# Performance work log

Measured on AMD Instinct MI355X. Metric: run time of the kernel, lower is better.

The kernel has to match this reference:

```python
import jax, jax.numpy as jnp
import numpy as np
import math

B, T, C, H, L, V = 8, 511, 1024, 16, 8, 128  # T = block_size - 1
D = C // H
FF = 4 * C


def setup_inputs() -> dict:
    key = jax.random.key(0)
    ks = jax.random.split(key, 12)
    std = 0.02
    n = lambda k, s: (jax.random.normal(k, s, dtype=jnp.float32) * std)
    idx = jax.random.randint(ks[0], (B, T), 0, V)
    idx = jnp.where(idx == 2, 3, idx)  # avoid pad token so logits[idx!=2] keeps all rows
    return {
        "idx": idx,
        "tok_emb": n(ks[1], (V, C)),
        "pos_emb": n(ks[2], (T, C)),
        "ln1_w": jnp.ones((L, C)), "ln1_b": jnp.zeros((L, C)),
        "Wq": n(ks[3], (L, C, C)), "bq": jnp.zeros((L, C)),
        "Wk": n(ks[4], (L, C, C)), "bk": jnp.zeros((L, C)),
        "Wv": n(ks[5], (L, C, C)), "bv": jnp.zeros((L, C)),
        "Wp": n(ks[6], (L, C, C)), "bp": jnp.zeros((L, C)),
        "ln2_w": jnp.ones((L, C)), "ln2_b": jnp.zeros((L, C)),
        "W1": n(ks[7], (L, C, FF)), "b1": jnp.zeros((L, FF)),
        "W2": n(ks[8], (L, FF, C)), "b2": jnp.zeros((L, C)),
        "lnf_w": jnp.ones((C,)), "lnf_b": jnp.zeros((C,)),
        "head_w": n(ks[9], (V, C)),
    }


def _ln(x, w, b):
    m = x.mean(-1, keepdims=True)
    v = ((x - m) ** 2).mean(-1, keepdims=True)
    return (x - m) * jax.lax.rsqrt(v + 1e-5) * w + b


def reference(idx, tok_emb, pos_emb, ln1_w, ln1_b, Wq, bq, Wk, bk, Wv, bv, Wp, bp,
              ln2_w, ln2_b, W1, b1, W2, b2, lnf_w, lnf_b, head_w):
    x = tok_emb[idx] + pos_emb[None, :, :]                      # [B,T,C]
    mask = jnp.tril(jnp.ones((T, T), dtype=bool))
    scale = 1.0 / math.sqrt(D)

    def block(x, p):
        h = _ln(x, p["ln1_w"], p["ln1_b"])
        q = (h @ p["Wq"] + p["bq"]).reshape(B, T, H, D).transpose(0, 2, 1, 3)
        k = (h @ p["Wk"] + p["bk"]).reshape(B, T, H, D).transpose(0, 2, 1, 3)
        v = (h @ p["Wv"] + p["bv"]).reshape(B, T, H, D).transpose(0, 2, 1, 3)
        att = jnp.einsum('bhqd,bhkd->bhqk', q, k) * scale       # [B,H,T,T]
        att = jnp.where(mask, att, -jnp.inf)
        att = jax.nn.softmax(att, axis=-1)
        y = jnp.einsum('bhqk,bhkd->bhqd', att, v)
        y = y.transpose(0, 2, 1, 3).reshape(B, T, C)
        x = x + y @ p["Wp"] + p["bp"]
        h = _ln(x, p["ln2_w"], p["ln2_b"])
        h = jax.nn.gelu(h @ p["W1"] + p["b1"], approximate=False)
        x = x + h @ p["W2"] + p["b2"]
        return x, None

    stacked = dict(ln1_w=ln1_w, ln1_b=ln1_b, Wq=Wq, bq=bq, Wk=Wk, bk=bk, Wv=Wv, bv=bv,
                   Wp=Wp, bp=bp, ln2_w=ln2_w, ln2_b=ln2_b, W1=W1, b1=b1, W2=W2, b2=b2)
    x, _ = jax.lax.scan(block, x, stacked)
    x = _ln(x, lnf_w, lnf_b)
    logits = x @ head_w.T                                       # [B,T,V]
    # logits[idx != 2] with no 2-tokens present == all rows flattened
    return logits.reshape(B * T, V)
```

## Files before the change

kernel.cpp:

```cpp
#include <hip/hip_runtime.h>
#include <hip/hip_bf16.h>

typedef unsigned short u16;
typedef unsigned int   u32;
typedef __attribute__((ext_vector_type(8))) __bf16 bf16x8;
typedef __attribute__((ext_vector_type(4))) float  f32x4;

static constexpr int NB  = 8;
static constexpr int TT  = 511;
static constexpr int CC  = 1024;
static constexpr int HH  = 16;
static constexpr int LL  = 8;
static constexpr int VV  = 128;
static constexpr int FF_ = 4096;
static constexpr int MV  = NB * TT;
static constexpr int MP  = 4096;
static constexpr int TP  = 512;

#define DEVI static __device__ __forceinline__

DEVI u16 f2bf(float f) {
  u32 u = __builtin_bit_cast(u32, f);
  u = (u + 0x7fffu + ((u >> 16) & 1u)) >> 16;
  return (u16)u;
}

DEVI void gload16(const void* g, void* lds) {
  auto gp = (const __attribute__((address_space(1))) u32*)(uintptr_t)g;
  auto lp = (__attribute__((address_space(3))) u32*)(uintptr_t)lds;
  __builtin_amdgcn_global_load_lds(gp, lp, 16, 0, 0);
}

__global__ __launch_bounds__(256) void k_transpose(const float* __restrict__ in,
                                                   u16* __restrict__ out, int K, int N,
                                                   size_t is, size_t os) {
  in  += (size_t)blockIdx.z * is;
  out += (size_t)blockIdx.z * os;
  __shared__ u16 tile[64][66];
  int nb = blockIdx.x * 64, kb = blockIdx.y * 64;
  int t = threadIdx.x;
  int r = t >> 4, c4 = (t & 15) * 4;
#pragma unroll
  for (int i = 0; i < 4; ++i) {
    int k = r + i * 16;
    float4 v = *(const float4*)(in + (size_t)(kb + k) * N + nb + c4);
    tile[k][c4 + 0] = f2bf(v.x); tile[k][c4 + 1] = f2bf(v.y);
    tile[k][c4 + 2] = f2bf(v.z); tile[k][c4 + 3] = f2bf(v.w);
  }
  __syncthreads();
#pragma unroll
  for (int i = 0; i < 4; ++i) {
    int n = r + i * 16;
    ushort4 o;
    o.x = tile[c4 + 0][n]; o.y = tile[c4 + 1][n];
    o.z = tile[c4 + 2][n]; o.w = tile[c4 + 3][n];
    *(ushort4*)(out + (size_t)(nb + n) * K + kb + c4) = o;
  }
}

__global__ __launch_bounds__(256) void k_transpose4(const float* __restrict__ Wq,
                                                    const float* __restrict__ Wk,
                                                    const float* __restrict__ Wv,
                                                    const float* __restrict__ Wp,
                                                    u16* __restrict__ wqkv_t,
                                                    u16* __restrict__ wp_t) {
  int z = blockIdx.z, which = z >> 3, lyr = z & 7;
  const float* in; u16* out;
  size_t sq = (size_t)CC * CC;
  if (which == 0)      { in = Wq + lyr * sq; out = wqkv_t + lyr * 3 * sq; }
  else if (which == 1) { in = Wk + lyr * sq; out = wqkv_t + lyr * 3 * sq + sq; }
  else if (which == 2) { in = Wv + lyr * sq; out = wqkv_t + lyr * 3 * sq + 2 * sq; }
  else                 { in = Wp + lyr * sq; out = wp_t + lyr * sq; }
  __shared__ u16 tile[64][66];
  int nb = blockIdx.x * 64, kb = blockIdx.y * 64;
  int t = threadIdx.x;
  int r = t >> 4, c4 = (t & 15) * 4;
#pragma unroll
  for (int i = 0; i < 4; ++i) {
    int k = r + i * 16;
    float4 v = *(const float4*)(in + (size_t)(kb + k) * CC + nb + c4);
    tile[k][c4 + 0] = f2bf(v.x); tile[k][c4 + 1] = f2bf(v.y);
    tile[k][c4 + 2] = f2bf(v.z); tile[k][c4 + 3] = f2bf(v.w);
  }
  __syncthreads();
#pragma unroll
  for (int i = 0; i < 4; ++i) {
    int n = r + i * 16;
    ushort4 o;
    o.x = tile[c4 + 0][n]; o.y = tile[c4 + 1][n];
    o.z = tile[c4 + 2][n]; o.w = tile[c4 + 3][n];
    *(ushort4*)(out + (size_t)(nb + n) * CC + kb + c4) = o;
  }
}

__global__ __launch_bounds__(256) void k_prep(const float* __restrict__ headw,
                                              const float* __restrict__ bq,
                                              const float* __restrict__ bk,
                                              const float* __restrict__ bv,
                                              u16* __restrict__ headb,
                                              float* __restrict__ bqkv) {
  int i = blockIdx.x * 256 + threadIdx.x;
  if (i < VV * CC) {
    headb[i] = f2bf(headw[i]);
  } else {
    int j = i - VV * CC;
    if (j < LL * 3 * CC) {
      int l = j / (3 * CC), c = j % (3 * CC);
      float v = (c < CC) ? bq[l * CC + c] : (c < 2 * CC) ? bk[l * CC + c - CC] : bv[l * CC + c - 2 * CC];
      bqkv[j] = v;
    }
  }
}

__global__ __launch_bounds__(256) void k_embed(const int* __restrict__ idx,
                                               const float* __restrict__ tok,
                                               const float* __restrict__ pos,
                                               float* __restrict__ x) {
  int row = blockIdx.x;
  int c4 = threadIdx.x * 4;
  if (row >= MV) {
    *(float4*)(x + (size_t)row * CC + c4) = make_float4(0.f, 0.f, 0.f, 0.f);
    return;
  }
  int t = row % TT;
  int tid = idx[row];
  float4 a = *(const float4*)(tok + (size_t)tid * CC + c4);
  float4 p = *(const float4*)(pos + (size_t)t * CC + c4);
  a.x += p.x; a.y += p.y; a.z += p.z; a.w += p.w;
  *(float4*)(x + (size_t)row * CC + c4) = a;
}

__global__ __launch_bounds__(256) void k_ln(const float* __restrict__ x,
                                            const float* __restrict__ w,
                                            const float* __restrict__ b,
                                            u16* __restrict__ out) {
  int wid = threadIdx.x >> 6, l = threadIdx.x & 63;
  int row = blockIdx.x * 4 + wid;
  const float* xr = x + (size_t)row * CC;
  float4 v[4];
  float s = 0.f, sq = 0.f;
#pragma unroll
  for (int i = 0; i < 4; ++i) {
    v[i] = *(const float4*)(xr + (i * 64 + l) * 4);
    s  += v[i].x + v[i].y + v[i].z + v[i].w;
    sq += v[i].x * v[i].x + v[i].y * v[i].y + v[i].z * v[i].z + v[i].w * v[i].w;
  }
#pragma unroll
  for (int o = 32; o; o >>= 1) { s += __shfl_xor(s, o); sq += __shfl_xor(sq, o); }
  float mean = s * (1.f / CC);
  float var  = sq * (1.f / CC) - mean * mean;
  float rs = rsqrtf(var + 1e-5f);
#pragma unroll
  for (int i = 0; i < 4; ++i) {
    int c = (i * 64 + l) * 4;
    float4 wv = *(const float4*)(w + c);
    float4 bv = *(const float4*)(b + c);
    ushort4 o4;
    o4.x = f2bf((v[i].x - mean) * rs * wv.x + bv.x);
    o4.y = f2bf((v[i].y - mean) * rs * wv.y + bv.y);
    o4.z = f2bf((v[i].z - mean) * rs * wv.z + bv.z);
    o4.w = f2bf((v[i].w - mean) * rs * wv.w + bv.w);
    *(ushort4*)(out + (size_t)row * CC + c) = o4;
  }
}

template <int EPI>
__global__ __launch_bounds__(512, 1) void k_gemm4(const u16* __restrict__ A,
                                                  const u16* __restrict__ Wt,
                                                  const float* __restrict__ bias,
                                                  u16* __restrict__ outb,
                                                  u16* __restrict__ vt,
                                                  int N, int K, int gridN) {
  __shared__ char lds[2][4][16384];
  int t = threadIdx.x, l = t & 63, wid = t >> 6;
  int wr = wid >> 2, wc = wid & 3;
  int lr = l & 15, lk16 = (l >> 4) * 16;

  int nwg = gridDim.x, wg = blockIdx.x;
  int qq = nwg >> 3, r8 = nwg & 7;
  int xcd = wg & 7, loc = wg >> 3;
  int swz = (xcd < r8 ? xcd * (qq + 1) : r8 * (qq + 1) + (xcd - r8) * qq) + loc;
  int mblk = swz / gridN, nblk = swz - mblk * gridN;
  int mb = mblk * 256, nb = nblk * 256;
  int NT = K >> 6;
  const u16* Ab = A  + (size_t)mb * K;
  const u16* Bb = Wt + (size_t)nb * K;

  int srow = t >> 3, skb = (t & 7) * 16;

  auto stageH = [&](int kt, int ht) {
    int b = kt & 1;
    const u16* src = (ht < 2) ? Ab : Bb;
    int rowbase = (ht & 1) << 7;
    char* dst = &lds[b][ht][0];
    const u16* s0 = src + (size_t)rowbase * K + kt * 64;
#pragma unroll
    for (int j = 0; j < 2; ++j) {
      int row = j * 64 + srow;
      int kb = skb ^ ((row & 7) << 4);
      gload16(s0 + (size_t)row * K + (kb >> 1), dst + j * 8192 + t * 16);
    }
  };

  f32x4 acc[8][4] = {};

  stageH(0, 0); stageH(0, 1); stageH(0, 2); stageH(0, 3);
  stageH(1, 2); stageH(1, 0); stageH(1, 3);
  asm volatile("s_waitcnt vmcnt(6)" ::: "memory");
  __builtin_amdgcn_s_barrier();
  __builtin_amdgcn_sched_barrier(0);

  for (int kt = 0; kt < NT; kt += 2) {
    bool s2 = (kt + 2) < NT, s3 = (kt + 3) < NT;
#pragma unroll
    for (int half = 0; half < 2; ++half) {
      int buf = half;
      bf16x8 Bf[2][4];
#pragma unroll
      for (int q = 0; q < 4; ++q) {
        bf16x8 Af[2][2];
        if (q == 0) {
#pragma unroll
          for (int ks = 0; ks < 2; ++ks)
#pragma unroll
            for (int nf = 0; nf < 4; ++nf) {
              int grow = ((wc & 1) << 6) + nf * 16 + lr;
              int kb = (ks * 64 + lk16) ^ ((grow & 7) << 4);
              Bf[ks][nf] = *(const bf16x8*)(&lds[buf][2 + (wc >> 1)][0] + grow * 128 + kb);
            }
        }
#pragma unroll
        for (int ks = 0; ks < 2; ++ks)
#pragma unroll
          for (int dm = 0; dm < 2; ++dm) {
            int mf = q * 2 + dm;
            int grow = wr * 64 + (mf & 3) * 16 + lr;
            int kb = (ks * 64 + lk16) ^ ((grow & 7) << 4);
            Af[ks][dm] = *(const bf16x8*)(&lds[buf][mf >> 2][0] + grow * 128 + kb);
          }
        if (half == 0) {
          if (q == 0)      stageH(kt + 1, 1);
          else if (q == 1) { if (s2) stageH(kt + 2, 2); }
          else if (q == 2) { if (s2) stageH(kt + 2, 0); }
          else             { if (s2) stageH(kt + 2, 3); }
        } else {
          if (q == 0)      { if (s2) stageH(kt + 2, 1); }
          else if (q == 1) { if (s3) stageH(kt + 3, 2); }
          else if (q == 2) { if (s3) stageH(kt + 3, 0); }
          else             { if (s3) stageH(kt + 3, 3); }
        }
        __builtin_amdgcn_sched_barrier(0);
        __builtin_amdgcn_s_barrier();
        asm volatile("s_waitcnt lgkmcnt(0)" ::: "memory");
        __builtin_amdgcn_sched_barrier(0);
        __builtin_amdgcn_s_setprio(1);
#pragma unroll
        for (int ks = 0; ks < 2; ++ks)
#pragma unroll
          for (int dm = 0; dm < 2; ++dm)
#pragma unroll
            for (int nf = 0; nf < 4; ++nf)
              acc[q * 2 + dm][nf] = __builtin_amdgcn_mfma_f32_16x16x32_bf16(
                  Af[ks][dm], Bf[ks][nf], acc[q * 2 + dm][nf], 0, 0, 0);
        __builtin_amdgcn_s_setprio(0);
        if (q == 3) {
          if (half == 0) {
            if (s2) asm volatile("s_waitcnt vmcnt(6)" ::: "memory");
            else    asm volatile("s_waitcnt vmcnt(0)" ::: "memory");
          } else if (s2) {
            if (s3) asm volatile("s_waitcnt vmcnt(6)" ::: "memory");
            else    asm volatile("s_waitcnt vmcnt(0)" ::: "memory");
          }
        }
        __builtin_amdgcn_sched_barrier(0);
        __builtin_amdgcn_s_barrier();
      }
    }
  }

  int r0 = (l >> 4) * 4;
#pragma unroll
  for (int mf = 0; mf < 8; ++mf) {
    int gr = mb + ((mf >> 2) << 7) + wr * 64 + (mf & 3) * 16 + r0;
#pragma unroll
    for (int nf = 0; nf < 4; ++nf) {
      int gc = nb + wc * 64 + nf * 16 + lr;
      float bv = bias[gc];
      if constexpr (EPI == 1) {
        if (gc >= 2048) {
          int h = (gc - 2048) >> 6, d = gc & 63;
#pragma unroll
          for (int rr = 0; rr < 4; ++rr) {
            int grow = gr + rr;
            if (grow < MV) {
              int b = grow / TT;
              int tt2 = grow - b * TT;
              vt[(((size_t)(b * HH + h)) * 64 + d) * TP + tt2] = f2bf(acc[mf][nf][rr] + bv);
            }
          }
          continue;
        }
      }
#pragma unroll
      for (int rr = 0; rr < 4; ++rr) {
        float v = acc[mf][nf][rr] + bv;
        size_t o = (size_t)(gr + rr) * N + gc;
        if constexpr (EPI == 1) {
          outb[o] = f2bf(v);
        } else {
          float g = 0.5f * v * (1.0f + erff(v * 0.70710678f));
          outb[o] = f2bf(g);
        }
      }
    }
  }
}

template <int EPI>
__global__ __launch_bounds__(256, 2) void k_gemm3(const u16* __restrict__ A,
                                                  const u16* __restrict__ Wt,
                                                  const float* __restrict__ bias,
                                                  float* __restrict__ outf,
                                                  const float* __restrict__ resid,
                                                  int N, int K, int gridN, int Mv) {
  constexpr int BTILE = 16384;
  __shared__ u16 lds[2][128 * 64 * 2];

  int t = threadIdx.x, l = t & 63, wid = t >> 6;
  int wr = wid >> 1, wc = wid & 1;
  int lr = l & 15, lk16 = (l >> 4) * 16;

  int nwg = gridDim.x, wg = blockIdx.x;
  int q = nwg >> 3, r = nwg & 7;
  int xcd = wg & 7, loc = wg >> 3;
  int swz = (xcd < r ? xcd * (q + 1) : r * (q + 1) + (xcd - r) * q) + loc;
  int mblk = swz / gridN;
  int nblk = swz - mblk * gridN;
  int mb = mblk * 128, nb = nblk * 128;
  int NT = K >> 6;
  const u16* Ab = A  + (size_t)mb * K;
  const u16* Bb = Wt + (size_t)nb * K;

  int srow = t >> 3;
  int skb  = (t & 7) * 16;

  auto stage = [&](int kt, int b) {
    const u16* As = Ab + kt * 64;
    char* LD = (char*)&lds[b][0];
#pragma unroll
    for (int j = 0; j < 4; ++j) {
      int row = j * 32 + srow;
      int kb  = skb ^ ((row & 7) << 4);
      gload16(As + (size_t)row * K + (kb >> 1), LD + j * 4096 + t * 16);
    }
    const u16* Bs = Bb + kt * 64;
#pragma unroll
    for (int j = 0; j < 4; ++j) {
      int row = j * 32 + srow;
      int kb  = skb ^ ((row & 7) << 4);
      gload16(Bs + (size_t)row * K + (kb >> 1), LD + BTILE + j * 4096 + t * 16);
    }
  };

  f32x4 acc[4][4] = {};

  auto tile = [&](int b) {
    const char* LA = (const char*)&lds[b][0];
    const char* LB = LA + BTILE;
    bf16x8 bfr[2][4], afr[2][4];
#pragma unroll
    for (int ks = 0; ks < 2; ++ks)
#pragma unroll
      for (int n = 0; n < 4; ++n) {
        int rr = wc * 64 + n * 16 + lr;
        int kb = (ks * 64 + lk16) ^ ((rr & 7) << 4);
        bfr[ks][n] = *(const bf16x8*)(LB + rr * 128 + kb);
      }
#pragma unroll
    for (int ks = 0; ks < 2; ++ks)
#pragma unroll
      for (int m = 0; m < 4; ++m) {
        int rr = wr * 64 + m * 16 + lr;
        int kb = (ks * 64 + lk16) ^ ((rr & 7) << 4);
        afr[ks][m] = *(const bf16x8*)(LA + rr * 128 + kb);
      }
    __builtin_amdgcn_s_setprio(1);
#pragma unroll
    for (int ks = 0; ks < 2; ++ks)
#pragma unroll
      for (int m = 0; m < 4; ++m)
#pragma unroll
        for (int n = 0; n < 4; ++n)
          acc[m][n] = __builtin_amdgcn_mfma_f32_16x16x32_bf16(
              afr[ks][m], bfr[ks][n], acc[m][n], 0, 0, 0);
    __builtin_amdgcn_s_setprio(0);
  };

  stage(0, 0);
  stage(1, 1);
  asm volatile("s_waitcnt vmcnt(8)" ::: "memory");
  __builtin_amdgcn_s_barrier();
  __builtin_amdgcn_sched_barrier(0);

  for (int kt = 0; kt < NT; kt += 2) {
#pragma unroll
    for (int sub = 0; sub < 2; ++sub) {
      tile(sub);
      asm volatile("s_waitcnt lgkmcnt(0)" ::: "memory");
      __builtin_amdgcn_s_barrier();
      __builtin_amdgcn_sched_barrier(0);
      if (kt + 2 + sub < NT) {
        stage(kt + 2 + sub, sub);
        asm volatile("s_waitcnt vmcnt(8)" ::: "memory");
      } else {
        asm volatile("s_waitcnt vmcnt(0)" ::: "memory");
      }
      __builtin_amdgcn_s_barrier();
      __builtin_amdgcn_sched_barrier(0);
    }
  }

  int r0 = (l >> 4) * 4;
#pragma unroll
  for (int m = 0; m < 4; ++m) {
    int gr = mb + wr * 64 + m * 16 + r0;
#pragma unroll
    for (int n = 0; n < 4; ++n) {
      int gc = nb + wc * 64 + n * 16 + lr;
      float bv = 0.f;
      if constexpr (EPI == 0) bv = bias[gc];
#pragma unroll
      for (int rr = 0; rr < 4; ++rr) {
        int grr = gr + rr;
        float v = acc[m][n][rr] + bv;
        size_t o = (size_t)grr * N + gc;
        if constexpr (EPI == 0) {
          outf[o] = v + resid[o];
        } else {
          if (grr < Mv) outf[o] = v;
        }
      }
    }
  }
}

__global__ __launch_bounds__(512, 2) void k_attn2(const u16* __restrict__ qkv,
                                                  const u16* __restrict__ vt,
                                                  u16* __restrict__ y) {
  __shared__ u16 Kb[2][64 * 64];
  __shared__ u16 Vb[2][64 * 64];
  __shared__ u16 Pb[8][16 * 64];
  int t = threadIdx.x, l = t & 63, w = t >> 6;

  int nwg = gridDim.x, wg = blockIdx.x;
  int swz = (wg & 7) * (nwg >> 3) + (wg >> 3);
  int bh = swz >> 2, qt = swz & 3;
  int b = bh >> 4, h = bh & 15;
  int q0 = qt * 128;
  int lr = l & 15, lg = l >> 4, lk8 = lg * 8;

  const float ISC = 0.125f;

  bf16x8 Qa[2];
  {
    int qs = q0 + w * 16 + lr;
    const u16* qp = qkv + (size_t)(b * TT + (qs < TT ? qs : TT - 1)) * 3072 + h * 64;
    Qa[0] = *(const bf16x8*)(qp + lk8);
    Qa[1] = *(const bf16x8*)(qp + 32 + lk8);
  }

  int NT = (q0 + 128) >> 6;

  int srow = w * 8 + (l >> 3);
  int sb16 = (l & 7) * 16;
  int bcol = sb16 ^ ((srow & 7) << 4);
  const u16* Ksrc = qkv + 1024 + h * 64;
  const char* Vsrc = (const char*)(vt + ((size_t)bh * 64 + srow) * TP);

  auto stage = [&](int kt, int buf) {
    int kv0 = kt * 64;
    int kvr = kv0 + srow;
    int krow = b * TT + (kvr < TT ? kvr : TT - 1);
    gload16((const char*)(Ksrc + (size_t)krow * 3072) + bcol, (char*)&Kb[buf][0] + t * 16);
    gload16(Vsrc + kv0 * 2 + bcol, (char*)&Vb[buf][0] + t * 16);
  };

  f32x4 O[4] = {};
  float m_[4], s_[4];
#pragma unroll
  for (int r = 0; r < 4; ++r) { m_[r] = -1e30f; s_[r] = 0.f; }

  stage(0, 0);
  for (int kt = 0; kt < NT; ++kt) {
    int buf = kt & 1;
    if (kt + 1 < NT) {
      stage(kt + 1, buf ^ 1);
      asm volatile("s_waitcnt vmcnt(2)" ::: "memory");
    } else {
      asm volatile("s_waitcnt vmcnt(0)" ::: "memory");
    }
    __builtin_amdgcn_s_barrier();

    int kv0 = kt * 64;
    f32x4 S[4];
    const char* LK = (const char*)&Kb[buf][0];
#pragma unroll
    for (int j = 0; j < 4; ++j) {
      f32x4 a = {};
#pragma unroll
      for (int ks = 0; ks < 2; ++ks) {
        int row = j * 16 + lr;
        int kb = ((ks * 32 + lk8) * 2) ^ ((row & 7) << 4);
        bf16x8 kf = *(const bf16x8*)(LK + row * 128 + kb);
        a = __builtin_amdgcn_mfma_f32_16x16x32_bf16(Qa[ks], kf, a, 0, 0, 0);
      }
      S[j] = a;
    }
    int qbase = q0 + w * 16 + lg * 4;
#pragma unroll
    for (int j = 0; j < 4; ++j) {
      int kv = kv0 + j * 16 + lr;
#pragma unroll
      for (int r = 0; r < 4; ++r) {
        bool valid = (kv <= qbase + r) && (kv < TT);
        S[j][r] = valid ? S[j][r] : -1e30f;
      }
    }
    float mx[4];
#pragma unroll
    for (int r = 0; r < 4; ++r)
      mx[r] = fmaxf(fmaxf(S[0][r], S[1][r]), fmaxf(S[2][r], S[3][r]));
#pragma unroll
    for (int r = 0; r < 4; ++r) {
      mx[r] = fmaxf(mx[r], __shfl_xor(mx[r], 1));
      mx[r] = fmaxf(mx[r], __shfl_xor(mx[r], 2));
      mx[r] = fmaxf(mx[r], __shfl_xor(mx[r], 4));
      mx[r] = fmaxf(mx[r], __shfl_xor(mx[r], 8));
    }
    float sc[4];
#pragma unroll
    for (int r = 0; r < 4; ++r) {
      float mn = fmaxf(m_[r], mx[r]);
      sc[r] = __expf((m_[r] - mn) * ISC);
      m_[r] = mn;
      s_[r] *= sc[r];
    }
#pragma unroll
    for (int j = 0; j < 4; ++j)
#pragma unroll
      for (int r = 0; r < 4; ++r) O[j][r] *= sc[r];
    float rs[4] = {0.f, 0.f, 0.f, 0.f};
    char* LP = (char*)&Pb[w][0];
#pragma unroll
    for (int j = 0; j < 4; ++j) {
#pragma unroll
      for (int r = 0; r < 4; ++r) {
        float p = __expf((S[j][r] - m_[r]) * ISC);
        rs[r] += p;
        int row = lg * 4 + r;
        int addr = (row * 128 + (j * 16 + lr) * 2) ^ ((row & 7) << 4);
        *(u16*)(LP + addr) = f2bf(p);
      }
    }
#pragma unroll
    for (int r = 0; r < 4; ++r) {
      rs[r] += __shfl_xor(rs[r], 1);
      rs[r] += __shfl_xor(rs[r], 2);
      rs[r] += __shfl_xor(rs[r], 4);
      rs[r] += __shfl_xor(rs[r], 8);
      s_[r] += rs[r];
    }
    bf16x8 Pa[2];
#pragma unroll
    for (int ks = 0; ks < 2; ++ks) {
      int addr = (lr * 128 + (ks * 32 + lk8) * 2) ^ ((lr & 7) << 4);
      Pa[ks] = *(const bf16x8*)(LP + addr);
    }
    const char* LV = (const char*)&Vb[buf][0];
#pragma unroll
    for (int j = 0; j < 4; ++j) {
#pragma unroll
      for (int ks = 0; ks < 2; ++ks) {
        int row = j * 16 + lr;
        int kb = ((ks * 32 + lk8) * 2) ^ ((row & 7) << 4);
        bf16x8 vf = *(const bf16x8*)(LV + row * 128 + kb);
        O[j] = __builtin_amdgcn_mfma_f32_16x16x32_bf16(Pa[ks], vf, O[j], 0, 0, 0);
      }
    }
    asm volatile("s_waitcnt lgkmcnt(0)" ::: "memory");
    __builtin_amdgcn_s_barrier();
  }

  int qs0 = q0 + w * 16 + lg * 4;
#pragma unroll
  for (int r = 0; r < 4; ++r) {
    float inv = 1.0f / s_[r];
    int qs = qs0 + r;
    if (qs < TT) {
      u16* yp = y + (size_t)(b * TT + qs) * CC + h * 64;
#pragma unroll
      for (int j = 0; j < 4; ++j)
        yp[j * 16 + lr] = f2bf(O[j][r] * inv);
    }
  }
}

extern "C" void kernel_launch(void* const* d_in, const int* in_sizes, int n_in,
                              void* d_out, int out_size, void* d_ws, size_t ws_size,
                              hipStream_t stream) {
  (void)in_sizes; (void)n_in; (void)out_size; (void)ws_size;
  const int*   idx  = (const int*)  d_in[0];
  const float* tok  = (const float*)d_in[1];
  const float* pos  = (const float*)d_in[2];
  const float* ln1w = (const float*)d_in[3];
  const float* ln1b = (const float*)d_in[4];
  const float* Wq   = (const float*)d_in[5];
  const float* bq   = (const float*)d_in[6];
  const float* Wk   = (const float*)d_in[7];
  const float* bk   = (const float*)d_in[8];
  const float* Wv   = (const float*)d_in[9];
  const float* bv   = (const float*)d_in[10];
  const float* Wp   = (const float*)d_in[11];
  const float* bp   = (const float*)d_in[12];
  const float* ln2w = (const float*)d_in[13];
  const float* ln2b = (const float*)d_in[14];
  const float* W1   = (const float*)d_in[15];
  const float* b1   = (const float*)d_in[16];
  const float* W2   = (const float*)d_in[17];
  const float* b2   = (const float*)d_in[18];
  const float* lnfw = (const float*)d_in[19];
  const float* lnfb = (const float*)d_in[20];
  const float* headw= (const float*)d_in[21];
  float* out = (float*)d_out;

  char* p = (char*)d_ws;
  auto alloc = [&](size_t bytes) { char* r = p; p += (bytes + 255) & ~(size_t)255; return r; };
  u16*   wqkv_t = (u16*)  alloc((size_t)LL * 3 * CC * CC * 2);
  u16*   wp_t   = (u16*)  alloc((size_t)LL * CC * CC * 2);
  u16*   w1_t   = (u16*)  alloc((size_t)LL * FF_ * CC * 2);
  u16*   w2_t   = (u16*)  alloc((size_t)LL * CC * FF_ * 2);
  u16*   headb  = (u16*)  alloc((size_t)VV * CC * 2);
  float* bqkv   = (float*)alloc((size_t)LL * 3 * CC * 4);
  float* x      = (float*)alloc((size_t)MP * CC * 4);
  u16*   hbuf   = (u16*)  alloc((size_t)MP * CC * 2);
  u16*   qkv    = (u16*)  alloc((size_t)MP * 3 * CC * 2);
  u16*   vt     = (u16*)  alloc((size_t)NB * HH * 64 * TP * 2);
  u16*   ybuf   = (u16*)  alloc((size_t)MP * CC * 2);
  u16*   ffb    = (u16*)  alloc((size_t)MP * FF_ * 2);

  k_transpose4<<<dim3(16, 16, 4 * LL), 256, 0, stream>>>(Wq, Wk, Wv, Wp, wqkv_t, wp_t);
  k_transpose<<<dim3(64, 16, LL), 256, 0, stream>>>(W1, w1_t, CC, FF_, (size_t)CC * FF_, (size_t)FF_ * CC);
  k_transpose<<<dim3(16, 64, LL), 256, 0, stream>>>(W2, w2_t, FF_, CC, (size_t)FF_ * CC, (size_t)CC * FF_);
  k_prep<<<(VV * CC + LL * 3 * CC + 255) / 256, 256, 0, stream>>>(headw, bq, bk, bv, headb, bqkv);

  k_embed<<<MP, 256, 0, stream>>>(idx, tok, pos, x);

  for (int l = 0; l < LL; ++l) {
    k_ln<<<MP / 4, 256, 0, stream>>>(x, ln1w + (size_t)l * CC, ln1b + (size_t)l * CC, hbuf);
    k_gemm4<1><<<12 * 16, 512, 0, stream>>>(hbuf, wqkv_t + (size_t)l * 3 * CC * CC,
                                            bqkv + (size_t)l * 3 * CC, qkv, vt, 3 * CC, CC, 12);
    k_attn2<<<NB * HH * 4, 512, 0, stream>>>(qkv, vt, ybuf);
    k_gemm3<0><<<32 * 8, 256, 0, stream>>>(ybuf, wp_t + (size_t)l * CC * CC,
                                           bp + (size_t)l * CC, x, x, CC, CC, 8, MP);
    k_ln<<<MP / 4, 256, 0, stream>>>(x, ln2w + (size_t)l * CC, ln2b + (size_t)l * CC, hbuf);
    k_gemm4<2><<<16 * 16, 512, 0, stream>>>(hbuf, w1_t + (size_t)l * FF_ * CC,
                                            b1 + (size_t)l * FF_, ffb, nullptr, FF_, CC, 16);
    k_gemm3<0><<<32 * 8, 256, 0, stream>>>(ffb, w2_t + (size_t)l * CC * FF_,
                                           b2 + (size_t)l * CC, x, x, CC, FF_, 8, MP);
  }

  k_ln<<<MP / 4, 256, 0, stream>>>(x, lnfw, lnfb, hbuf);
  k_gemm3<3><<<32 * 1, 256, 0, stream>>>(hbuf, headb, nullptr, out, nullptr, VV, CC, 1, MV);
}
```

Baseline: 1.840 ms.

## Split-K head GEMM, separate V transpose kernel, wider transpose stores

Replaces the 32-block head GEMM with an 8-way split-K GEMM that writes fp32 partials to a workspace buffer, followed by a reduction kernel. This fills more CUs for the small final projection. It also moves the scattered V-transpose writes out of the QKV GEMM epilogue into a dedicated LDS-tiled transpose kernel. The weight transpose kernels now store 16 bytes per thread instead of 8. These changes add extra launches and partial-buffer traffic, and the split-K path falls back to the old kernel if the workspace is too small.

```diff
diff --git a/kernel.cpp b/kernel.cpp
--- a/kernel.cpp
+++ b/kernel.cpp
@@ -5,6 +5,7 @@
 typedef unsigned int   u32;
 typedef __attribute__((ext_vector_type(8))) __bf16 bf16x8;
 typedef __attribute__((ext_vector_type(4))) float  f32x4;
+typedef __attribute__((ext_vector_type(8))) unsigned short u16x8;
 
 static constexpr int NB  = 8;
 static constexpr int TT  = 511;
@@ -16,6 +17,7 @@
 static constexpr int MV  = NB * TT;
 static constexpr int MP  = 4096;
 static constexpr int TP  = 512;
+static constexpr size_t PH = (size_t)MP * VV;
 
 #define DEVI static __device__ __forceinline__
 
@@ -48,13 +50,14 @@
     tile[k][c4 + 2] = f2bf(v.z); tile[k][c4 + 3] = f2bf(v.w);
   }
   __syncthreads();
-#pragma unroll
-  for (int i = 0; i < 4; ++i) {
-    int n = r + i * 16;
-    ushort4 o;
-    o.x = tile[c4 + 0][n]; o.y = tile[c4 + 1][n];
-    o.z = tile[c4 + 2][n]; o.w = tile[c4 + 3][n];
-    *(ushort4*)(out + (size_t)(nb + n) * K + kb + c4) = o;
+  int k8 = (t & 7) * 8;
+#pragma unroll
+  for (int i = 0; i < 2; ++i) {
+    int n = (t >> 3) + i * 32;
+    u16x8 o;
+#pragma unroll
+    for (int j = 0; j < 8; ++j) o[j] = tile[k8 + j][n];
+    *(u16x8*)(out + (size_t)(nb + n) * K + kb + k8) = o;
   }
 }
 
@@ -83,13 +86,14 @@
     tile[k][c4 + 2] = f2bf(v.z); tile[k][c4 + 3] = f2bf(v.w);
   }
   __syncthreads();
-#pragma unroll
-  for (int i = 0; i < 4; ++i) {
-    int n = r + i * 16;
-    ushort4 o;
-    o.x = tile[c4 + 0][n]; o.y = tile[c4 + 1][n];
-    o.z = tile[c4 + 2][n]; o.w = tile[c4 + 3][n];
-    *(ushort4*)(out + (size_t)(nb + n) * CC + kb + c4) = o;
+  int k8 = (t & 7) * 8;
+#pragma unroll
+  for (int i = 0; i < 2; ++i) {
+    int n = (t >> 3) + i * 32;
+    u16x8 o;
+#pragma unroll
+    for (int j = 0; j < 8; ++j) o[j] = tile[k8 + j][n];
+    *(u16x8*)(out + (size_t)(nb + n) * CC + kb + k8) = o;
   }
 }
 
@@ -169,7 +173,6 @@
                                                   const u16* __restrict__ Wt,
                                                   const float* __restrict__ bias,
                                                   u16* __restrict__ outb,
-                                                  u16* __restrict__ vt,
                                                   int N, int K, int gridN) {
   __shared__ char lds[2][4][16384];
   int t = threadIdx.x, l = t & 63, wid = t >> 6;
@@ -286,21 +289,6 @@
     for (int nf = 0; nf < 4; ++nf) {
       int gc = nb + wc * 64 + nf * 16 + lr;
       float bv = bias[gc];
-      if constexpr (EPI == 1) {
-        if (gc >= 2048) {
-          int h = (gc - 2048) >> 6, d = gc & 63;
-#pragma unroll
-          for (int rr = 0; rr < 4; ++rr) {
-            int grow = gr + rr;
-            if (grow < MV) {
-              int b = grow / TT;
-              int tt2 = grow - b * TT;
-              vt[(((size_t)(b * HH + h)) * 64 + d) * TP + tt2] = f2bf(acc[mf][nf][rr] + bv);
-            }
-          }
-          continue;
-        }
-      }
 #pragma unroll
       for (int rr = 0; rr < 4; ++rr) {
         float v = acc[mf][nf][rr] + bv;
@@ -444,6 +432,161 @@
   }
 }
 
+__global__ __launch_bounds__(256, 2) void k_gemm3sk(const u16* __restrict__ A,
+                                                    const u16* __restrict__ Wt,
+                                                    float* __restrict__ pbuf,
+                                                    int N, int K) {
+  constexpr int KS = 8;
+  constexpr int BTILE = 16384;
+  __shared__ u16 lds[2][128 * 64 * 2];
+
+  int t = threadIdx.x, l = t & 63, wid = t >> 6;
+  int wr = wid >> 1, wc = wid & 1;
+  int lr = l & 15, lk16 = (l >> 4) * 16;
+
+  int nwg = gridDim.x, wg = blockIdx.x;
+  int q = nwg >> 3, r = nwg & 7;
+  int xcd = wg & 7, loc = wg >> 3;
+  int swz = (xcd < r ? xcd * (q + 1) : r * (q + 1) + (xcd - r) * q) + loc;
+  int mblk = swz / KS;
+  int kz   = swz - mblk * KS;
+  int mb = mblk * 128, nb = 0;
+  int Ksub = K / KS;
+  int NT = Ksub >> 6;
+  const u16* Ab = A  + (size_t)mb * K + (size_t)kz * Ksub;
+  const u16* Bb = Wt + (size_t)kz * Ksub;
+
+  int srow = t >> 3;
+  int skb  = (t & 7) * 16;
+
+  auto stage = [&](int kt, int b) {
+    const u16* As = Ab + kt * 64;
+    char* LD = (char*)&lds[b][0];
+#pragma unroll
+    for (int j = 0; j < 4; ++j) {
+      int row = j * 32 + srow;
+      int kb  = skb ^ ((row & 7) << 4);
+      gload16(As + (size_t)row * K + (kb >> 1), LD + j * 4096 + t * 16);
+    }
+    const u16* Bs = Bb + kt * 64;
+#pragma unroll
+    for (int j = 0; j < 4; ++j) {
+      int row = j * 32 + srow;
+      int kb  = skb ^ ((row & 7) << 4);
+      gload16(Bs + (size_t)row * K + (kb >> 1), LD + BTILE + j * 4096 + t * 16);
+    }
+  };
+
+  f32x4 acc[4][4] = {};
+
+  auto tile = [&](int b) {
+    const char* LA = (const char*)&lds[b][0];
+    const char* LB = LA + BTILE;
+    bf16x8 bfr[2][4], afr[2][4];
+#pragma unroll
+    for (int ks = 0; ks < 2; ++ks)
+#pragma unroll
+      for (int n = 0; n < 4; ++n) {
+        int rr = wc * 64 + n * 16 + lr;
+        int kb = (ks * 64 + lk16) ^ ((rr & 7) << 4);
+        bfr[ks][n] = *(const bf16x8*)(LB + rr * 128 + kb);
+      }
+#pragma unroll
+    for (int ks = 0; ks < 2; ++ks)
+#pragma unroll
+      for (int m = 0; m < 4; ++m) {
+        int rr = wr * 64 + m * 16 + lr;
+        int kb = (ks * 64 + lk16) ^ ((rr & 7) << 4);
+        afr[ks][m] = *(const bf16x8*)(LA + rr * 128 + kb);
+      }
+#pragma unroll
+    for (int ks = 0; ks < 2; ++ks)
+#pragma unroll
+      for (int m = 0; m < 4; ++m)
+#pragma unroll
+        for (int n = 0; n < 4; ++n)
+          acc[m][n] = __builtin_amdgcn_mfma_f32_16x16x32_bf16(
+              afr[ks][m], bfr[ks][n], acc[m][n], 0, 0, 0);
+  };
+
+  stage(0, 0);
+  stage(1, 1);
+  asm volatile("s_waitcnt vmcnt(8)" ::: "memory");
+  __builtin_amdgcn_s_barrier();
+  __builtin_amdgcn_sched_barrier(0);
+
+  for (int kt = 0; kt < NT; kt += 2) {
+#pragma unroll
+    for (int sub = 0; sub < 2; ++sub) {
+      tile(sub);
+      asm volatile("s_waitcnt lgkmcnt(0)" ::: "memory");
+      __builtin_amdgcn_s_barrier();
+      __builtin_amdgcn_sched_barrier(0);
+      if (kt + 2 + sub < NT) {
+        stage(kt + 2 + sub, sub);
+        asm volatile("s_waitcnt vmcnt(8)" ::: "memory");
+      } else {
+        asm volatile("s_waitcnt vmcnt(0)" ::: "memory");
+      }
+      __builtin_amdgcn_s_barrier();
+      __builtin_amdgcn_sched_barrier(0);
+    }
+  }
+
+  float* pb = pbuf + (size_t)kz * PH;
+  int r0 = (l >> 4) * 4;
+#pragma unroll
+  for (int m = 0; m < 4; ++m) {
+    int gr = mb + wr * 64 + m * 16 + r0;
+#pragma unroll
+    for (int n = 0; n < 4; ++n) {
+      int gc = nb + wc * 64 + n * 16 + lr;
+#pragma unroll
+      for (int rr = 0; rr < 4; ++rr)
+        pb[(size_t)(gr + rr) * N + gc] = acc[m][n][rr];
+    }
+  }
+}
+
+__global__ __launch_bounds__(256) void k_redhead(const float* __restrict__ pb,
+                                                 float* __restrict__ out) {
+  int i = blockIdx.x * 256 + threadIdx.x;
+  float s = 0.f;
+#pragma unroll
+  for (int z = 0; z < 8; ++z) s += pb[(size_t)z * PH + i];
+  out[i] = s;
+}
+
+__global__ __launch_bounds__(256) void k_vtrans(const u16* __restrict__ qkv,
+                                                u16* __restrict__ vt) {
+  __shared__ u16 tile[64][66];
+  int bh = blockIdx.y;
+  int b = bh >> 4, h = bh & 15;
+  int t0 = blockIdx.x * 64;
+  int t = threadIdx.x;
+  int r = t >> 4, c4 = (t & 15) * 4;
+#pragma unroll
+  for (int i = 0; i < 4; ++i) {
+    int tt = r + i * 16;
+    int trow = t0 + tt;
+    int srow = b * TT + (trow < TT ? trow : TT - 1);
+    ushort4 v = *(const ushort4*)(qkv + (size_t)srow * 3072 + 2048 + h * 64 + c4);
+    tile[tt][c4 + 0] = v.x; tile[tt][c4 + 1] = v.y;
+    tile[tt][c4 + 2] = v.z; tile[tt][c4 + 3] = v.w;
+  }
+  __syncthreads();
+#pragma unroll
+  for (int i = 0; i < 4; ++i) {
+    int d = r + i * 16;
+    ushort4 o;
+    o.x = (t0 + c4 + 0 < TT) ? tile[c4 + 0][d] : (u16)0;
+    o.y = (t0 + c4 + 1 < TT) ? tile[c4 + 1][d] : (u16)0;
+    o.z = (t0 + c4 + 2 < TT) ? tile[c4 + 2][d] : (u16)0;
+    o.w = (t0 + c4 + 3 < TT) ? tile[c4 + 3][d] : (u16)0;
+    *(ushort4*)(vt + ((size_t)bh * 64 + d) * TP + t0 + c4) = o;
+  }
+}
+
 __global__ __launch_bounds__(512, 2) void k_attn2(const u16* __restrict__ qkv,
                                                   const u16* __restrict__ vt,
                                                   u16* __restrict__ y) {
@@ -608,7 +751,7 @@
 extern "C" void kernel_launch(void* const* d_in, const int* in_sizes, int n_in,
                               void* d_out, int out_size, void* d_ws, size_t ws_size,
                               hipStream_t stream) {
-  (void)in_sizes; (void)n_in; (void)out_size; (void)ws_size;
+  (void)in_sizes; (void)n_in; (void)out_size;
   const int*   idx  = (const int*)  d_in[0];
   const float* tok  = (const float*)d_in[1];
   const float* pos  = (const float*)d_in[2];
@@ -647,6 +790,8 @@
   u16*   vt     = (u16*)  alloc((size_t)NB * HH * 64 * TP * 2);
   u16*   ybuf   = (u16*)  alloc((size_t)MP * CC * 2);
   u16*   ffb    = (u16*)  alloc((size_t)MP * FF_ * 2);
+  float* pbuf   = (float*)alloc((size_t)8 * PH * 4);
+  bool havePB = ((size_t)(p - (char*)d_ws) <= ws_size);
 
   k_transpose4<<<dim3(16, 16, 4 * LL), 256, 0, stream>>>(Wq, Wk, Wv, Wp, wqkv_t, wp_t);
   k_transpose<<<dim3(64, 16, LL), 256, 0, stream>>>(W1, w1_t, CC, FF_, (size_t)CC * FF_, (size_t)FF_ * CC);
@@ -654,21 +799,29 @@
   k_prep<<<(VV * CC + LL * 3 * CC + 255) / 256, 256, 0, stream>>>(headw, bq, bk, bv, headb, bqkv);
 
   k_embed<<<MP, 256, 0, stream>>>(idx, tok, pos, x);
+  k_ln<<<MP / 4, 256, 0, stream>>>(x, ln1w, ln1b, hbuf);
 
   for (int l = 0; l < LL; ++l) {
-    k_ln<<<MP / 4, 256, 0, stream>>>(x, ln1w + (size_t)l * CC, ln1b + (size_t)l * CC, hbuf);
+    const float* nw = (l < LL - 1) ? ln1w + (size_t)(l + 1) * CC : lnfw;
+    const float* nb = (l < LL - 1) ? ln1b + (size_t)(l + 1) * CC : lnfb;
     k_gemm4<1><<<12 * 16, 512, 0, stream>>>(hbuf, wqkv_t + (size_t)l * 3 * CC * CC,
-                                            bqkv + (size_t)l * 3 * CC, qkv, vt, 3 * CC, CC, 12);
+                                            bqkv + (size_t)l * 3 * CC, qkv, 3 * CC, CC, 12);
+    k_vtrans<<<dim3(8, NB * HH), 256, 0, stream>>>(qkv, vt);
     k_attn2<<<NB * HH * 4, 512, 0, stream>>>(qkv, vt, ybuf);
     k_gemm3<0><<<32 * 8, 256, 0, stream>>>(ybuf, wp_t + (size_t)l * CC * CC,
                                            bp + (size_t)l * CC, x, x, CC, CC, 8, MP);
     k_ln<<<MP / 4, 256, 0, stream>>>(x, ln2w + (size_t)l * CC, ln2b + (size_t)l * CC, hbuf);
     k_gemm4<2><<<16 * 16, 512, 0, stream>>>(hbuf, w1_t + (size_t)l * FF_ * CC,
-                                            b1 + (size_t)l * FF_, ffb, nullptr, FF_, CC, 16);
+                                            b1 + (size_t)l * FF_, ffb, FF_, CC, 16);
     k_gemm3<0><<<32 * 8, 256, 0, stream>>>(ffb, w2_t + (size_t)l * CC * FF_,
                                            b2 + (size_t)l * CC, x, x, CC, FF_, 8, MP);
-  }
-
-  k_ln<<<MP / 4, 256, 0, stream>>>(x, lnfw, lnfb, hbuf);
-  k_gemm3<3><<<32 * 1, 256, 0, stream>>>(hbuf, headb, nullptr, out, nullptr, VV, CC, 1, MV);
-}
+    k_ln<<<MP / 4, 256, 0, stream>>>(x, nw, nb, hbuf);
+  }
+
+  if (havePB) {
+    k_gemm3sk<<<32 * 8, 256, 0, stream>>>(hbuf, headb, pbuf, VV, CC);
+    k_redhead<<<(MV * VV) / 256, 256, 0, stream>>>(pbuf, out);
+  } else {
+    k_gemm3<3><<<32 * 1, 256, 0, stream>>>(hbuf, headb, nullptr, out, nullptr, VV, CC, 1, MV);
+  }
+}
```

New measurement: 1.683 ms. 8.5% less time.
